# Kernel optimization log

Hardware: AMD Instinct MI355X
Metric: run time of the kernel (lower is better)

## Reference

```python
import jax, jax.numpy as jnp
import numpy as np

INPUT_DIM = 768
STATE_DIM = 128
LN_EPS = 1e-5
CLAMP = 10.0


def setup_inputs() -> dict:
    key = jax.random.key(0)
    ks = jax.random.split(key, 9)
    B, T, D, S = 128, 256, INPUT_DIM, STATE_DIM
    x = jax.random.normal(ks[0], (B, T, D), dtype=jnp.float32)
    A = jax.random.normal(ks[1], (S, S), dtype=jnp.float32) * 0.01
    # nn.Linear weights are [out_features, in_features]
    B_w = jax.random.normal(ks[2], (S, D), dtype=jnp.float32) * (1.0 / np.sqrt(D))
    C_w = jax.random.normal(ks[3], (D, S), dtype=jnp.float32) * (1.0 / np.sqrt(S))
    D_w = jax.random.normal(ks[4], (D, D), dtype=jnp.float32) * (1.0 / np.sqrt(D))
    gate_w = jax.random.normal(ks[5], (2, D), dtype=jnp.float32) * (1.0 / np.sqrt(D))
    gate_b = jnp.zeros((2,), dtype=jnp.float32)
    ln_gamma = jnp.ones((D,), dtype=jnp.float32)
    ln_beta = jnp.zeros((D,), dtype=jnp.float32)
    return {"x": x, "A": A, "B_w": B_w, "C_w": C_w, "D_w": D_w,
            "gate_w": gate_w, "gate_b": gate_b,
            "ln_gamma": ln_gamma, "ln_beta": ln_beta}


def reference(x, A, B_w, C_w, D_w, gate_w, gate_b, ln_gamma, ln_beta):
    B, T, D = x.shape
    S = A.shape[0]
    residual = x
    # Precompute input projection for all timesteps: [B, T, S]
    Bx = jnp.einsum('btd,sd->bts', x, B_w)

    def step(state, bx_t):
        # state: [B, S]; state @ A.T + B(x_t), clamped
        state = jnp.clip(state @ A.T + bx_t, -CLAMP, CLAMP)
        return state, state

    init = jnp.zeros((B, S), dtype=x.dtype)
    _, states = jax.lax.scan(step, init, jnp.swapaxes(Bx, 0, 1))  # [T, B, S]
    states = jnp.swapaxes(states, 0, 1)  # [B, T, S]

    # Output projection (vectorized over all timesteps)
    out = jnp.einsum('bts,ds->btd', states, C_w) + jnp.einsum('btd,ed->bte', x, D_w)

    # Gating mix with residual
    gate = jax.nn.softmax(jnp.einsum('btd,gd->btg', x, gate_w) + gate_b, axis=-1)
    out = gate[..., 0:1] * out + gate[..., 1:2] * residual

    # LayerNorm (dropout is identity in eval)
    mu = jnp.mean(out, axis=-1, keepdims=True)
    var = jnp.var(out, axis=-1, keepdims=True)
    out = (out - mu) * jax.lax.rsqrt(var + LN_EPS) * ln_gamma + ln_beta
    return out
```

## Files before the change

### kernel.cpp

```cpp
#include <hip/hip_runtime.h>
#include <hip/hip_bf16.h>
#include <stdint.h>

typedef __bf16 bf16;
typedef __bf16 bf16x4 __attribute__((ext_vector_type(4)));
typedef __bf16 bf16x8 __attribute__((ext_vector_type(8)));
typedef float  f32x4  __attribute__((ext_vector_type(4)));

static constexpr int BB = 128;
static constexpr int TT = 256;
static constexpr int DD = 768;
static constexpr int SS = 128;
static constexpr int MM = BB * TT;
static constexpr int KW1 = DD + SS;

__device__ __forceinline__ void gload16(const void* g, void* l) {
  __builtin_amdgcn_global_load_lds(
      (const __attribute__((address_space(1))) void*)(uintptr_t)g,
      (__attribute__((address_space(3))) void*)(uintptr_t)l, 16, 0, 0);
}

__global__ __launch_bounds__(256) void k0_convert(
    const float* __restrict__ B_w, const float* __restrict__ D_w,
    const float* __restrict__ C_w, bf16* __restrict__ W0, bf16* __restrict__ W1) {
  int i = blockIdx.x * 256 + threadIdx.x;
  if (i < SS * DD) {
    W0[i] = (bf16)B_w[i];
  } else {
    int j = i - SS * DD;
    int n = j / KW1;
    int k = j - n * KW1;
    float v = (k < DD) ? D_w[n * DD + k] : C_w[n * SS + (k - DD)];
    W1[j] = (bf16)v;
  }
}

__global__ __launch_bounds__(256) void k0x_convert(
    const float* __restrict__ x, bf16* __restrict__ xb) {
  int i = blockIdx.x * 256 + threadIdx.x;
  const float4* src = (const float4*)x;
  float4 a = src[i * 2], b = src[i * 2 + 1];
  bf16x8 h;
  h[0] = (bf16)a.x; h[1] = (bf16)a.y; h[2] = (bf16)a.z; h[3] = (bf16)a.w;
  h[4] = (bf16)b.x; h[5] = (bf16)b.y; h[6] = (bf16)b.z; h[7] = (bf16)b.w;
  *(bf16x8*)&xb[i * 8] = h;
}

template <int TAG>
__global__ __launch_bounds__(256) void kg(
    const bf16* __restrict__ A1, const bf16* __restrict__ A2,
    const bf16* __restrict__ W, float* __restrict__ C,
    int kt1, int kt2, int lda1, int lda2, int ldb, int ldc) {
  __shared__ __align__(16) bf16 As[128 * 64];
  __shared__ __align__(16) bf16 Bs[128 * 64];

  const int tid = threadIdx.x;
  const int lane = tid & 63;
  const int wv = tid >> 6;
  const int wr = wv >> 1, wc = wv & 1;
  const int lr = lane & 15, lh = lane >> 4;
  const int bn0 = blockIdx.x * 128;
  const int bm0 = blockIdx.y * 128;

  const int l_row = lane >> 3;
  const int l_col = (lane & 7) * 8;

  f32x4 acc[4][4] = {};
  const int KT = kt1 + kt2;

  for (int kt = 0; kt < KT; ++kt) {
    __syncthreads();
    {
      const bf16* Ab;
      int lda;
      if (kt < kt1) { Ab = A1 + (size_t)bm0 * lda1 + kt * 64; lda = lda1; }
      else          { Ab = A2 + (size_t)bm0 * lda2 + (kt - kt1) * 64; lda = lda2; }
      #pragma unroll
      for (int it = 0; it < 4; ++it) {
        int c = wv * 4 + it;
        const bf16* g = Ab + (size_t)(c * 8 + l_row) * lda + l_col;
        gload16(g, &As[c * 512]);
      }
    }
    {
      const bf16* Bb = W + (size_t)bn0 * ldb + kt * 64;
      #pragma unroll
      for (int it = 0; it < 4; ++it) {
        int c = wv * 4 + it;
        const bf16* g = Bb + (size_t)(c * 8 + l_row) * ldb + l_col;
        gload16(g, &Bs[c * 512]);
      }
    }
    __syncthreads();
    #pragma unroll
    for (int kk = 0; kk < 2; ++kk) {
      bf16x8 af[4], bfr[4];
      #pragma unroll
      for (int f = 0; f < 4; ++f)
        af[f] = *(const bf16x8*)&As[(wr * 64 + f * 16 + lr) * 64 + kk * 32 + lh * 8];
      #pragma unroll
      for (int f = 0; f < 4; ++f)
        bfr[f] = *(const bf16x8*)&Bs[(wc * 64 + f * 16 + lr) * 64 + kk * 32 + lh * 8];
      #pragma unroll
      for (int fi = 0; fi < 4; ++fi)
        #pragma unroll
        for (int fj = 0; fj < 4; ++fj)
          acc[fi][fj] = __builtin_amdgcn_mfma_f32_16x16x32_bf16(
              af[fi], bfr[fj], acc[fi][fj], 0, 0, 0);
    }
  }
  #pragma unroll
  for (int fi = 0; fi < 4; ++fi)
    #pragma unroll
    for (int fj = 0; fj < 4; ++fj) {
      int row = bm0 + wr * 64 + fi * 16 + lh * 4;
      int col = bn0 + wc * 64 + fj * 16 + lr;
      float* Cp = C + (size_t)row * ldc + col;
      #pragma unroll
      for (int r = 0; r < 4; ++r) Cp[(size_t)r * ldc] = acc[fi][fj][r];
    }
}

__global__ __launch_bounds__(256) void k_gemm(
    const float* __restrict__ A1, const bf16* __restrict__ A2,
    const bf16* __restrict__ W, float* __restrict__ C,
    int kt1, int kt2, int lda1, int lda2, int ldb, int ldc) {
  __shared__ __align__(16) bf16 As[128][72];
  __shared__ __align__(16) bf16 Bs[128][72];

  const int tid = threadIdx.x;
  const int lane = tid & 63;
  const int wv = tid >> 6;
  const int wr = wv >> 1, wc = wv & 1;
  const int lr = lane & 15, lh = lane >> 4;
  const int bn0 = blockIdx.x * 128;
  const int bm0 = blockIdx.y * 128;

  f32x4 acc[4][4] = {};
  const int KT = kt1 + kt2;

  for (int kt = 0; kt < KT; ++kt) {
    __syncthreads();
    if (kt < kt1) {
      const float* Ab = A1 + (size_t)bm0 * lda1 + kt * 64;
      #pragma unroll
      for (int it = 0; it < 8; ++it) {
        int c = it * 256 + tid;
        int row = c >> 4, col = (c & 15) << 2;
        float4 v = *(const float4*)(Ab + (size_t)row * lda1 + col);
        bf16x4 h;
        h[0] = (bf16)v.x; h[1] = (bf16)v.y; h[2] = (bf16)v.z; h[3] = (bf16)v.w;
        *(bf16x4*)&As[row][col] = h;
      }
    } else {
      const bf16* Ab = A2 + (size_t)bm0 * lda2 + (kt - kt1) * 64;
      #pragma unroll
      for (int it = 0; it < 8; ++it) {
        int c = it * 256 + tid;
        int row = c >> 4, col = (c & 15) << 2;
        bf16x4 v = *(const bf16x4*)(Ab + (size_t)row * lda2 + col);
        *(bf16x4*)&As[row][col] = v;
      }
    }
    {
      const bf16* Bb = W + (size_t)bn0 * ldb + kt * 64;
      #pragma unroll
      for (int it = 0; it < 8; ++it) {
        int c = it * 256 + tid;
        int row = c >> 4, col = (c & 15) << 2;
        bf16x4 v = *(const bf16x4*)(Bb + (size_t)row * ldb + col);
        *(bf16x4*)&Bs[row][col] = v;
      }
    }
    __syncthreads();
    #pragma unroll
    for (int kk = 0; kk < 2; ++kk) {
      bf16x8 af[4], bfr[4];
      #pragma unroll
      for (int f = 0; f < 4; ++f)
        af[f] = *(const bf16x8*)&As[wr * 64 + f * 16 + lr][kk * 32 + lh * 8];
      #pragma unroll
      for (int f = 0; f < 4; ++f)
        bfr[f] = *(const bf16x8*)&Bs[wc * 64 + f * 16 + lr][kk * 32 + lh * 8];
      #pragma unroll
      for (int fi = 0; fi < 4; ++fi)
        #pragma unroll
        for (int fj = 0; fj < 4; ++fj)
          acc[fi][fj] = __builtin_amdgcn_mfma_f32_16x16x32_bf16(
              af[fi], bfr[fj], acc[fi][fj], 0, 0, 0);
    }
  }
  #pragma unroll
  for (int fi = 0; fi < 4; ++fi)
    #pragma unroll
    for (int fj = 0; fj < 4; ++fj) {
      int row = bm0 + wr * 64 + fi * 16 + lh * 4;
      int col = bn0 + wc * 64 + fj * 16 + lr;
      float* Cp = C + (size_t)row * ldc + col;
      #pragma unroll
      for (int r = 0; r < 4; ++r) Cp[(size_t)r * ldc] = acc[fi][fj][r];
    }
}

__global__ __launch_bounds__(512) void k2_scan(
    const float* __restrict__ Bx, const float* __restrict__ A,
    bf16* __restrict__ states) {
  __shared__ __align__(16) float st[2][SS];
  __shared__ __align__(16) float part[3][SS];
  __shared__ __align__(16) float bxb[2][32 * SS];

  const int tid = threadIdx.x;
  const int s = tid & 127;
  const int q = tid >> 7;
  const int b = blockIdx.x;

  float areg[32];
  {
    const float* Ar = A + s * SS + q * 32;
    #pragma unroll
    for (int j = 0; j < 8; ++j) {
      float4 v = *(const float4*)(Ar + j * 4);
      areg[j * 4 + 0] = v.x; areg[j * 4 + 1] = v.y;
      areg[j * 4 + 2] = v.z; areg[j * 4 + 3] = v.w;
    }
  }
  if (tid < SS) st[0][tid] = 0.f;

  const float* Bxb = Bx + (size_t)b * TT * SS;
  {
    float4 c0 = *(const float4*)(Bxb + tid * 4);
    float4 c1 = *(const float4*)(Bxb + 2048 + tid * 4);
    *(float4*)&bxb[0][tid * 4] = c0;
    *(float4*)&bxb[0][2048 + tid * 4] = c1;
  }
  float4 n0 = *(const float4*)(Bxb + 4096 + tid * 4);
  float4 n1 = *(const float4*)(Bxb + 4096 + 2048 + tid * 4);
  __syncthreads();

  bf16* so = states + (size_t)b * TT * SS;
  int p = 0, cur = 0;
  for (int ch = 0; ch < 8; ++ch) {
    #pragma unroll 1
    for (int t2 = 0; t2 < 32; ++t2) {
      const float* stp = st[p];
      float a0 = 0.f, a1 = 0.f, a2 = 0.f, a3 = 0.f;
      #pragma unroll
      for (int j = 0; j < 32; j += 4) {
        float4 sv = *(const float4*)(stp + (q << 5) + j);
        a0 += areg[j]     * sv.x;
        a1 += areg[j + 1] * sv.y;
        a2 += areg[j + 2] * sv.z;
        a3 += areg[j + 3] * sv.w;
      }
      float partial = (a0 + a1) + (a2 + a3);
      if (q) part[q - 1][s] = partial;
      __syncthreads();
      if (q == 0) {
        float tot = partial + part[0][s] + part[1][s] + part[2][s]
                  + bxb[cur][t2 * SS + s];
        tot = fminf(10.f, fmaxf(-10.f, tot));
        st[p ^ 1][s] = tot;
        so[(size_t)(ch * 32 + t2) * SS + s] = (bf16)tot;
      }
      __syncthreads();
      p ^= 1;
    }
    if (ch < 7) {
      *(float4*)&bxb[cur ^ 1][tid * 4] = n0;
      *(float4*)&bxb[cur ^ 1][2048 + tid * 4] = n1;
      if (ch < 6) {
        n0 = *(const float4*)(Bxb + (ch + 2) * 4096 + tid * 4);
        n1 = *(const float4*)(Bxb + (ch + 2) * 4096 + 2048 + tid * 4);
      }
      __syncthreads();
      cur ^= 1;
    }
  }
}

__global__ __launch_bounds__(256) void k4_epilogue(
    float* __restrict__ out, const float* __restrict__ x,
    const float* __restrict__ gate_w, const float* __restrict__ gate_b,
    const float* __restrict__ ln_g, const float* __restrict__ ln_b) {
  const int lane = threadIdx.x & 63;
  const int w = threadIdx.x >> 6;
  const int r = blockIdx.x * 4 + w;

  float4* orow = (float4*)(out + (size_t)r * DD);
  const float4* xrow = (const float4*)(x + (size_t)r * DD);
  const float4* g0w = (const float4*)gate_w;
  const float4* g1w = (const float4*)(gate_w + DD);

  float4 o[3], xv[3];
  float d = 0.f;
  #pragma unroll
  for (int i = 0; i < 3; ++i) {
    int c = i * 64 + lane;
    o[i] = orow[c];
    xv[i] = xrow[c];
    float4 w0 = g0w[c], w1 = g1w[c];
    d += xv[i].x * (w0.x - w1.x) + xv[i].y * (w0.y - w1.y)
       + xv[i].z * (w0.z - w1.z) + xv[i].w * (w0.w - w1.w);
  }
  #pragma unroll
  for (int off = 32; off > 0; off >>= 1) d += __shfl_xor(d, off);
  d += gate_b[0] - gate_b[1];
  float g0 = 1.f / (1.f + expf(-d));
  float g1 = 1.f - g0;

  float4 m[3];
  float s1 = 0.f, s2 = 0.f;
  #pragma unroll
  for (int i = 0; i < 3; ++i) {
    m[i].x = g0 * o[i].x + g1 * xv[i].x;
    m[i].y = g0 * o[i].y + g1 * xv[i].y;
    m[i].z = g0 * o[i].z + g1 * xv[i].z;
    m[i].w = g0 * o[i].w + g1 * xv[i].w;
    s1 += (m[i].x + m[i].y) + (m[i].z + m[i].w);
    s2 += (m[i].x * m[i].x + m[i].y * m[i].y)
        + (m[i].z * m[i].z + m[i].w * m[i].w);
  }
  #pragma unroll
  for (int off = 32; off > 0; off >>= 1) {
    s1 += __shfl_xor(s1, off);
    s2 += __shfl_xor(s2, off);
  }
  float mu = s1 * (1.f / 768.f);
  float var = s2 * (1.f / 768.f) - mu * mu;
  float rs = rsqrtf(var + 1e-5f);

  #pragma unroll
  for (int i = 0; i < 3; ++i) {
    int c = i * 64 + lane;
    float4 gg = ((const float4*)ln_g)[c];
    float4 bb = ((const float4*)ln_b)[c];
    float4 y;
    y.x = (m[i].x - mu) * rs * gg.x + bb.x;
    y.y = (m[i].y - mu) * rs * gg.y + bb.y;
    y.z = (m[i].z - mu) * rs * gg.z + bb.z;
    y.w = (m[i].w - mu) * rs * gg.w + bb.w;
    orow[c] = y;
  }
}

extern "C" void kernel_launch(void* const* d_in, const int* in_sizes, int n_in,
                              void* d_out, int out_size, void* d_ws, size_t ws_size,
                              hipStream_t stream) {
  const float* x   = (const float*)d_in[0];
  const float* A   = (const float*)d_in[1];
  const float* B_w = (const float*)d_in[2];
  const float* C_w = (const float*)d_in[3];
  const float* D_w = (const float*)d_in[4];
  const float* gw  = (const float*)d_in[5];
  const float* gb  = (const float*)d_in[6];
  const float* lng = (const float*)d_in[7];
  const float* lnb = (const float*)d_in[8];
  float* out = (float*)d_out;

  bf16* W0 = (bf16*)d_ws;
  bf16* W1 = W0 + SS * DD;
  bf16* states = W1 + DD * KW1;
  bf16* xb = states + (size_t)MM * SS;
  const size_t ws_need =
      2ull * (SS * DD + DD * KW1 + (size_t)MM * SS + (size_t)MM * DD);
  float* Bx = out + ((size_t)MM * DD - (size_t)MM * SS);

  k0_convert<<<dim3(3072), dim3(256), 0, stream>>>(B_w, D_w, C_w, W0, W1);

  if (ws_size >= ws_need) {
    k0x_convert<<<dim3(12288), dim3(256), 0, stream>>>(x, xb);
    kg<1><<<dim3(1, 256), dim3(256), 0, stream>>>(
        xb, (const bf16*)nullptr, W0, Bx, 12, 0, DD, 0, DD, SS);
    k2_scan<<<dim3(128), dim3(512), 0, stream>>>(Bx, A, states);
    kg<3><<<dim3(6, 256), dim3(256), 0, stream>>>(
        xb, states, W1, out, 12, 2, DD, SS, KW1, DD);
  } else {
    k_gemm<<<dim3(1, 256), dim3(256), 0, stream>>>(
        x, (const bf16*)nullptr, W0, Bx, 12, 0, DD, 0, DD, SS);
    k2_scan<<<dim3(128), dim3(512), 0, stream>>>(Bx, A, states);
    k_gemm<<<dim3(6, 256), dim3(256), 0, stream>>>(
        x, states, W1, out, 12, 2, DD, SS, KW1, DD);
  }

  k4_epilogue<<<dim3(8192), dim3(256), 0, stream>>>(out, x, gw, gb, lng, lnb);
}
```

Measured before the change: 404.2 us.

## Overlap recurrent scan with x·D_w GEMM in one fused launch

The serial state scan now runs in the same launch as the x·D_w part of the output GEMM: the first 128 blocks do per-batch recurrences while the remaining 1536 blocks compute out = x·D_wᵀ. The scan now uses 256 threads with A rows held in registers, reads Bx as bf16 written by the first GEMM, and writes states back in place. A small final GEMM adds states·C_wᵀ into out with an accumulate mode. This is meant to hide the latency-bound scan behind GEMM work, at the cost of bf16 rounding of Bx, an extra read-modify-write pass over out, and a possible scheduling risk if the scan blocks are not dispatched early.

```diff
diff --git a/kernel.cpp b/kernel.cpp
--- a/kernel.cpp
+++ b/kernel.cpp
@@ -49,8 +49,8 @@
 template <int TAG>
 __global__ __launch_bounds__(256) void kg(
     const bf16* __restrict__ A1, const bf16* __restrict__ A2,
-    const bf16* __restrict__ W, float* __restrict__ C,
-    int kt1, int kt2, int lda1, int lda2, int ldb, int ldc) {
+    const bf16* __restrict__ W, void* __restrict__ Cv,
+    int kt1, int kt2, int lda1, int lda2, int ldb, int ldc, int mode) {
   __shared__ __align__(16) bf16 As[128 * 64];
   __shared__ __align__(16) bf16 Bs[128 * 64];
 
@@ -71,15 +71,13 @@
   for (int kt = 0; kt < KT; ++kt) {
     __syncthreads();
     {
-      const bf16* Ab;
-      int lda;
+      const bf16* Ab; int lda;
       if (kt < kt1) { Ab = A1 + (size_t)bm0 * lda1 + kt * 64; lda = lda1; }
       else          { Ab = A2 + (size_t)bm0 * lda2 + (kt - kt1) * 64; lda = lda2; }
       #pragma unroll
       for (int it = 0; it < 4; ++it) {
         int c = wv * 4 + it;
-        const bf16* g = Ab + (size_t)(c * 8 + l_row) * lda + l_col;
-        gload16(g, &As[c * 512]);
+        gload16(Ab + (size_t)(c * 8 + l_row) * lda + l_col, &As[c * 512]);
       }
     }
     {
@@ -87,8 +85,7 @@
       #pragma unroll
       for (int it = 0; it < 4; ++it) {
         int c = wv * 4 + it;
-        const bf16* g = Bb + (size_t)(c * 8 + l_row) * ldb + l_col;
-        gload16(g, &Bs[c * 512]);
+        gload16(Bb + (size_t)(c * 8 + l_row) * ldb + l_col, &Bs[c * 512]);
       }
     }
     __syncthreads();
@@ -115,10 +112,167 @@
     for (int fj = 0; fj < 4; ++fj) {
       int row = bm0 + wr * 64 + fi * 16 + lh * 4;
       int col = bn0 + wc * 64 + fj * 16 + lr;
-      float* Cp = C + (size_t)row * ldc + col;
-      #pragma unroll
-      for (int r = 0; r < 4; ++r) Cp[(size_t)r * ldc] = acc[fi][fj][r];
-    }
+      if (mode == 0) {
+        float* Cp = (float*)Cv + (size_t)row * ldc + col;
+        #pragma unroll
+        for (int r = 0; r < 4; ++r) Cp[(size_t)r * ldc] = acc[fi][fj][r];
+      } else if (mode == 1) {
+        bf16* Cp = (bf16*)Cv + (size_t)row * ldc + col;
+        #pragma unroll
+        for (int r = 0; r < 4; ++r) Cp[(size_t)r * ldc] = (bf16)acc[fi][fj][r];
+      } else {
+        float* Cp = (float*)Cv + (size_t)row * ldc + col;
+        #pragma unroll
+        for (int r = 0; r < 4; ++r) Cp[(size_t)r * ldc] += acc[fi][fj][r];
+      }
+    }
+}
+
+__global__ __launch_bounds__(256) void k_fused(
+    const bf16* __restrict__ xb, const bf16* __restrict__ W1,
+    float* __restrict__ out, bf16* SB, const float* __restrict__ A) {
+  __shared__ __align__(16) char sraw[34304];
+
+  if (blockIdx.x < 128) {
+    float* st   = (float*)sraw;
+    float* part = (float*)(sraw + 1024);
+    float* bxb  = (float*)(sraw + 1536);
+
+    const int tid = threadIdx.x;
+    const int s = tid & 127;
+    const int q = tid >> 7;
+    bf16* Bxb = SB + (size_t)blockIdx.x * TT * SS;
+
+    float areg[64];
+    {
+      const float* Ar = A + s * SS + q * 64;
+      #pragma unroll
+      for (int j = 0; j < 16; ++j) {
+        float4 v = *(const float4*)(Ar + j * 4);
+        areg[j * 4 + 0] = v.x; areg[j * 4 + 1] = v.y;
+        areg[j * 4 + 2] = v.z; areg[j * 4 + 3] = v.w;
+      }
+    }
+    if (tid < SS) st[tid] = 0.f;
+
+    {
+      bf16x8 c0 = *(const bf16x8*)(Bxb + tid * 16);
+      bf16x8 c1 = *(const bf16x8*)(Bxb + tid * 16 + 8);
+      float* d0 = &bxb[tid * 16];
+      #pragma unroll
+      for (int e = 0; e < 8; ++e) d0[e] = (float)c0[e];
+      #pragma unroll
+      for (int e = 0; e < 8; ++e) d0[8 + e] = (float)c1[e];
+    }
+    bf16x8 n0 = *(const bf16x8*)(Bxb + 4096 + tid * 16);
+    bf16x8 n1 = *(const bf16x8*)(Bxb + 4096 + tid * 16 + 8);
+    __syncthreads();
+
+    int p = 0, cur = 0;
+    for (int ch = 0; ch < 8; ++ch) {
+      #pragma unroll 1
+      for (int t2 = 0; t2 < 32; ++t2) {
+        const float* stp = st + p * SS;
+        float a0 = 0.f, a1 = 0.f, a2 = 0.f, a3 = 0.f;
+        #pragma unroll
+        for (int j = 0; j < 64; j += 4) {
+          float4 sv = *(const float4*)(stp + (q << 6) + j);
+          a0 += areg[j]     * sv.x;
+          a1 += areg[j + 1] * sv.y;
+          a2 += areg[j + 2] * sv.z;
+          a3 += areg[j + 3] * sv.w;
+        }
+        float partial = (a0 + a1) + (a2 + a3);
+        if (q) part[s] = partial;
+        __syncthreads();
+        if (!q) {
+          float tot = partial + part[s] + bxb[cur * 4096 + t2 * SS + s];
+          tot = fminf(10.f, fmaxf(-10.f, tot));
+          st[(p ^ 1) * SS + s] = tot;
+          Bxb[(size_t)(ch * 32 + t2) * SS + s] = (bf16)tot;
+        }
+        __syncthreads();
+        p ^= 1;
+      }
+      if (ch < 7) {
+        float* dn = &bxb[(cur ^ 1) * 4096 + tid * 16];
+        #pragma unroll
+        for (int e = 0; e < 8; ++e) dn[e] = (float)n0[e];
+        #pragma unroll
+        for (int e = 0; e < 8; ++e) dn[8 + e] = (float)n1[e];
+        if (ch < 6) {
+          n0 = *(const bf16x8*)(Bxb + (ch + 2) * 4096 + tid * 16);
+          n1 = *(const bf16x8*)(Bxb + (ch + 2) * 4096 + tid * 16 + 8);
+        }
+        __syncthreads();
+        cur ^= 1;
+      }
+    }
+  } else {
+    bf16* As = (bf16*)sraw;
+    bf16* Bs = (bf16*)(sraw + 16384);
+
+    const int gb = blockIdx.x - 128;
+    const int bn0 = (gb % 6) * 128;
+    const int bm0 = (gb / 6) * 128;
+
+    const int tid = threadIdx.x;
+    const int lane = tid & 63;
+    const int wv = tid >> 6;
+    const int wr = wv >> 1, wc = wv & 1;
+    const int lr = lane & 15, lh = lane >> 4;
+    const int l_row = lane >> 3;
+    const int l_col = (lane & 7) * 8;
+
+    f32x4 acc[4][4] = {};
+
+    for (int kt = 0; kt < 12; ++kt) {
+      __syncthreads();
+      {
+        const bf16* Ab = xb + (size_t)bm0 * DD + kt * 64;
+        #pragma unroll
+        for (int it = 0; it < 4; ++it) {
+          int c = wv * 4 + it;
+          gload16(Ab + (size_t)(c * 8 + l_row) * DD + l_col, &As[c * 512]);
+        }
+      }
+      {
+        const bf16* Bb = W1 + (size_t)bn0 * KW1 + kt * 64;
+        #pragma unroll
+        for (int it = 0; it < 4; ++it) {
+          int c = wv * 4 + it;
+          gload16(Bb + (size_t)(c * 8 + l_row) * KW1 + l_col, &Bs[c * 512]);
+        }
+      }
+      __syncthreads();
+      #pragma unroll
+      for (int kk = 0; kk < 2; ++kk) {
+        bf16x8 af[4], bfr[4];
+        #pragma unroll
+        for (int f = 0; f < 4; ++f)
+          af[f] = *(const bf16x8*)&As[(wr * 64 + f * 16 + lr) * 64 + kk * 32 + lh * 8];
+        #pragma unroll
+        for (int f = 0; f < 4; ++f)
+          bfr[f] = *(const bf16x8*)&Bs[(wc * 64 + f * 16 + lr) * 64 + kk * 32 + lh * 8];
+        #pragma unroll
+        for (int fi = 0; fi < 4; ++fi)
+          #pragma unroll
+          for (int fj = 0; fj < 4; ++fj)
+            acc[fi][fj] = __builtin_amdgcn_mfma_f32_16x16x32_bf16(
+                af[fi], bfr[fj], acc[fi][fj], 0, 0, 0);
+      }
+    }
+    #pragma unroll
+    for (int fi = 0; fi < 4; ++fi)
+      #pragma unroll
+      for (int fj = 0; fj < 4; ++fj) {
+        int row = bm0 + wr * 64 + fi * 16 + lh * 4;
+        int col = bn0 + wc * 64 + fj * 16 + lr;
+        float* Cp = out + (size_t)row * DD + col;
+        #pragma unroll
+        for (int r = 0; r < 4; ++r) Cp[(size_t)r * DD] = acc[fi][fj][r];
+      }
+  }
 }
 
 __global__ __launch_bounds__(256) void k_gemm(
@@ -359,24 +513,26 @@
 
   bf16* W0 = (bf16*)d_ws;
   bf16* W1 = W0 + SS * DD;
-  bf16* states = W1 + DD * KW1;
-  bf16* xb = states + (size_t)MM * SS;
-  const size_t ws_need =
+  bf16* SB = W1 + DD * KW1;
+  bf16* xb = SB + (size_t)MM * SS;
+  const size_t ws_need_fast =
       2ull * (SS * DD + DD * KW1 + (size_t)MM * SS + (size_t)MM * DD);
-  float* Bx = out + ((size_t)MM * DD - (size_t)MM * SS);
+  const size_t ws_need_min = 2ull * (SS * DD + DD * KW1 + (size_t)MM * SS);
 
   k0_convert<<<dim3(3072), dim3(256), 0, stream>>>(B_w, D_w, C_w, W0, W1);
 
-  if (ws_size >= ws_need) {
+  if (ws_size >= ws_need_fast) {
     k0x_convert<<<dim3(12288), dim3(256), 0, stream>>>(x, xb);
     kg<1><<<dim3(1, 256), dim3(256), 0, stream>>>(
-        xb, (const bf16*)nullptr, W0, Bx, 12, 0, DD, 0, DD, SS);
-    k2_scan<<<dim3(128), dim3(512), 0, stream>>>(Bx, A, states);
+        xb, nullptr, W0, SB, 12, 0, DD, 0, DD, SS, 1);
+    k_fused<<<dim3(128 + 1536), dim3(256), 0, stream>>>(xb, W1, out, SB, A);
     kg<3><<<dim3(6, 256), dim3(256), 0, stream>>>(
-        xb, states, W1, out, 12, 2, DD, SS, KW1, DD);
-  } else {
+        SB, nullptr, W1 + DD, out, 2, 0, SS, 0, KW1, DD, 2);
+  } else if (ws_size >= ws_need_min) {
+    float* Bx = out + ((size_t)MM * DD - (size_t)MM * SS);
+    bf16* states = SB;
     k_gemm<<<dim3(1, 256), dim3(256), 0, stream>>>(
-        x, (const bf16*)nullptr, W0, Bx, 12, 0, DD, 0, DD, SS);
+        x, nullptr, W0, Bx, 12, 0, DD, 0, DD, SS);
     k2_scan<<<dim3(128), dim3(512), 0, stream>>>(Bx, A, states);
     k_gemm<<<dim3(6, 256), dim3(256), 0, stream>>>(
         x, states, W1, out, 12, 2, DD, SS, KW1, DD);
```

After: 436.2 us. +7.9%, slower.
